# Performance work log

Hardware: AMD Instinct MI355X
Metric: run time of the kernel (lower is better)

## Reference

```python
import jax, jax.numpy as jnp
import numpy as np

B, T, XD, ZD, H = 1024, 1000, 8, 8, 256


def setup_inputs() -> dict:
    key = jax.random.key(0)
    ks = jax.random.split(key, 10)
    # monotonically increasing time grid, identical per batch element: [B, T, 1]
    t = jnp.broadcast_to(jnp.linspace(0.0, 10.0, T, dtype=jnp.float32)[None, :, None], (B, T, 1))
    x = jax.random.normal(ks[0], (B, T, XD), jnp.float32)
    z = jax.random.normal(ks[1], (B, T, ZD), jnp.float32)
    event_t = jax.random.uniform(ks[2], (B, 1), jnp.float32, 3.0, 7.0)
    z_jump = jax.random.normal(ks[3], (B, ZD), jnp.float32)
    in_dim = 3 * (XD + ZD)

    def lin(k, fan_in, fan_out):
        return jax.random.normal(k, (fan_in, fan_out), jnp.float32) * (1.0 / np.sqrt(fan_in))

    W1 = lin(ks[4], in_dim, H); b1 = jnp.zeros((H,), jnp.float32)
    W2 = lin(ks[5], H, H);     b2 = jnp.zeros((H,), jnp.float32)
    W3 = lin(ks[6], H, H);     b3 = jnp.zeros((H,), jnp.float32)
    W4 = lin(ks[7], H, XD);    b4 = jnp.zeros((XD,), jnp.float32)
    return dict(t=t, x=x, z=z, event_t=event_t, z_jump=z_jump,
                W1=W1, b1=b1, W2=W2, b2=b2, W3=W3, b3=b3, W4=W4, b4=b4)


def reference(t, x, z, event_t, z_jump, W1, b1, W2, b2, W3, b3, W4, b4):
    # all_initial = cat(x[:,0], z[:,0]) : [B, XD+ZD]
    all_initial = jnp.concatenate([x[:, 0], z[:, 0]], axis=-1)

    def de_func(x_cur, z_eff):
        xtzt = jnp.concatenate([x_cur, z_eff], axis=-1)                      # [B, XD+ZD]
        inp = jnp.concatenate([all_initial, xtzt - all_initial, xtzt], -1)   # [B, 3*(XD+ZD)]
        h = jax.nn.elu(inp @ W1 + b1)
        h = jax.nn.elu(h @ W2 + b2)
        h = jax.nn.elu(h @ W3 + b3)
        return h @ W4 + b4                                                   # [B, XD]

    t_seq = jnp.moveaxis(t, 1, 0)   # [T, B, 1]
    z_seq = jnp.moveaxis(z, 1, 0)   # [T, B, ZD]
    dt = t_seq[1:] - t_seq[:-1]     # [T-1, B, 1]

    def step(x_cur, step_in):
        t_i, dt_i, z_i = step_in
        # event: once t passes event_t, exogenous z jumps to z_jump
        z_eff = jnp.where(t_i >= event_t, z_jump, z_i)
        x_next = x_cur + dt_i * de_func(x_cur, z_eff)  # explicit Euler step
        return x_next, x_next

    x0 = x[:, 0]  # initial condition [B, XD]
    _, xs = jax.lax.scan(step, x0, (t_seq[:-1], dt, z_seq[:-1]))
    sol = jnp.concatenate([x0[None], xs], axis=0)  # [T, B, XD]
    return jnp.moveaxis(sol, 0, 1)                 # [B, T, XD]
```

## Files before the change

kernel.cpp:

```cpp
#include <hip/hip_runtime.h>
#include <cstdint>
#include <cstddef>

typedef __bf16 bf16x8 __attribute__((ext_vector_type(8)));
typedef float f32x4 __attribute__((ext_vector_type(4)));

#define HD 256
#define TLEN 1000
#define NSTEP 999

#define W1R_OFF 0
#define W2R_OFF 16384
#define W3R_OFF 81920
#define W4R_OFF 147456
#define WS_ELEMS 151552

__device__ __forceinline__ void wg_barrier() {
  asm volatile("s_waitcnt lgkmcnt(0)\n\ts_barrier" ::: "memory");
}

__global__ void prep_weights(const float* __restrict__ W1, const float* __restrict__ b1,
                             const float* __restrict__ W2, const float* __restrict__ W3,
                             const float* __restrict__ W4, __bf16* __restrict__ ws) {
  int tid = blockIdx.x * blockDim.x + threadIdx.x;
  if (tid >= WS_ELEMS) return;
  float val = 0.0f;
  if (tid < W2R_OFF) {
    int t = tid;
    int j = t & 7, lane = (t >> 3) & 63, tt = (t >> 9) & 1, kb = (t >> 10) & 1, w = (t >> 11) & 7;
    int k = kb * 32 + ((lane >> 4) * 8) + j;
    int n = w * 32 + tt * 16 + (lane & 15);
    if (k < 48) val = W1[k * HD + n];
    else if (k == 48) val = b1[n];
  } else if (tid < W3R_OFF) {
    int t = tid - W2R_OFF;
    int j = t & 7, lane = (t >> 3) & 63, tt = (t >> 9) & 1, kb = (t >> 10) & 7, w = (t >> 13) & 7;
    int k = kb * 32 + ((lane >> 4) * 8) + j;
    int n = w * 32 + tt * 16 + (lane & 15);
    val = W2[k * HD + n];
  } else if (tid < W4R_OFF) {
    int t = tid - W3R_OFF;
    int j = t & 7, lane = (t >> 3) & 63, tt = (t >> 9) & 1, kb = (t >> 10) & 7, w = (t >> 13) & 7;
    int k = kb * 32 + ((lane >> 4) * 8) + j;
    int n = w * 32 + tt * 16 + (lane & 15);
    val = W3[k * HD + n];
  } else {
    int t = tid - W4R_OFF;
    int j = t & 7, lane = (t >> 3) & 63, kb = (t >> 9) & 7;
    int k = kb * 32 + ((lane >> 4) * 8) + j;
    int n = lane & 15;
    val = (n < 8) ? W4[k * 8 + n] : 0.0f;
  }
  ws[tid] = (__bf16)val;
}

__global__ __launch_bounds__(512, 2) void ode_main(
    const float* __restrict__ t_g, const float* __restrict__ x_g,
    const float* __restrict__ z_g, const float* __restrict__ ev_g,
    const float* __restrict__ zj_g, const float* __restrict__ b2_g,
    const float* __restrict__ b3_g, const float* __restrict__ b4_g,
    const __bf16* __restrict__ ws, float* __restrict__ out) {
  __shared__ __align__(16) __bf16 h_a[16 * 264];
  __shared__ __align__(16) __bf16 h_b[16 * 264];
  __shared__ __align__(16) float p4[8 * 16 * 8];
  __shared__ __align__(16) float x_cur[16 * 12];
  __shared__ __align__(16) float z_eff[16 * 12];
  __shared__ __align__(16) float x0s[16 * 12];
  __shared__ __align__(16) float z0s[16 * 12];
  __shared__ __align__(16) float zjs[16 * 12];
  __shared__ float evs[16];

  const int tid  = threadIdx.x;
  const int lane = tid & 63;
  const int wid  = tid >> 6;
  const int bcol = lane & 15;
  const int q    = lane >> 4;
  const int b0   = blockIdx.x * 16;

  if (tid < 128) {
    int m = tid >> 3, d = tid & 7;
    size_t gb = (size_t)(b0 + m);
    float x0 = x_g[gb * (TLEN * 8) + d];
    float z0 = z_g[gb * (TLEN * 8) + d];
    x0s[m * 12 + d] = x0;
    z0s[m * 12 + d] = z0;
    x_cur[m * 12 + d] = x0;
    zjs[m * 12 + d] = zj_g[gb * 8 + d];
    out[gb * (TLEN * 8) + d] = x0;
    if (d == 0) evs[m] = ev_g[gb];
  }
  __syncthreads();

  if (tid < 128) {
    int m = tid >> 3, d = tid & 7;
    float t0 = t_g[0];
    z_eff[m * 12 + d] = (t0 >= evs[m]) ? zjs[m * 12 + d] : z0s[m * 12 + d];
  }

  const bf16x8* wsv = (const bf16x8*)ws;
  bf16x8 w1f[2][2], w2f[8][2], w3f[8][2];
#pragma unroll
  for (int kb = 0; kb < 2; ++kb)
#pragma unroll
    for (int tt = 0; tt < 2; ++tt)
      w1f[kb][tt] = wsv[(W1R_OFF / 8) + ((wid * 2 + kb) * 2 + tt) * 64 + lane];
#pragma unroll
  for (int kb = 0; kb < 8; ++kb)
#pragma unroll
    for (int tt = 0; tt < 2; ++tt) {
      w2f[kb][tt] = wsv[(W2R_OFF / 8) + ((wid * 8 + kb) * 2 + tt) * 64 + lane];
      w3f[kb][tt] = wsv[(W3R_OFF / 8) + ((wid * 8 + kb) * 2 + tt) * 64 + lane];
    }
  bf16x8 w4f = wsv[(W4R_OFF / 8) + wid * 64 + lane];

  f32x4 b2v[2], b3v[2];
#pragma unroll
  for (int tt = 0; tt < 2; ++tt) {
    int n0 = wid * 32 + tt * 16 + q * 4;
    b2v[tt] = *(const f32x4*)(b2_g + n0);
    b3v[tt] = *(const f32x4*)(b3_g + n0);
  }
  float b4l = (tid < 128) ? b4_g[tid & 7] : 0.0f;

  const int m1 = lane >> 2;
  const int d0 = (lane & 3) * 2;
  float2 zjf = make_float2(0.f, 0.f);
  float ev1 = 0.f;
  if (wid == 2) {
    zjf.x = zjs[m1 * 12 + d0];
    zjf.y = zjs[m1 * 12 + d0 + 1];
    ev1 = evs[m1];
  }

  f32x4 sub0, sub1;
  bf16x8 a0c;
  {
    const float* base = ((q & 1) ? z0s : x0s) + bcol * 12;
    f32x4 r0 = *(const f32x4*)(base);
    f32x4 r1 = *(const f32x4*)(base + 4);
    sub0 = r0; sub1 = r1;
#pragma unroll
    for (int e = 0; e < 4; ++e) { a0c[e] = (__bf16)r0[e]; a0c[e + 4] = (__bf16)r1[e]; }
  }
  bf16x8 zf;
#pragma unroll
  for (int e = 0; e < 8; ++e) zf[e] = (__bf16)0.f;
  bf16x8 k48f = zf;
  k48f[0] = (__bf16)1.0f;

  __syncthreads();

  float tc = t_g[0];

  auto layer = [&](const __bf16* src, __bf16* dst, const bf16x8 (*wf)[2], const f32x4* bv) {
    bf16x8 bfr[8];
    const bf16x8* hp = (const bf16x8*)src;
#pragma unroll
    for (int kb = 0; kb < 8; ++kb) bfr[kb] = hp[bcol * 33 + kb * 4 + q];
#pragma unroll
    for (int tt = 0; tt < 2; ++tt) {
      f32x4 c = bv[tt];
#pragma unroll
      for (int kb = 0; kb < 8; ++kb)
        c = __builtin_amdgcn_mfma_f32_16x16x32_bf16(wf[kb][tt], bfr[kb], c, 0, 0, 0);
      union { __bf16 h4[4]; unsigned long long u; } pk;
#pragma unroll
      for (int e = 0; e < 4; ++e) {
        float v = c[e];
        v = (v > 0.f) ? v : (__expf(v) - 1.0f);
        pk.h4[e] = (__bf16)v;
      }
      *(unsigned long long*)(dst + bcol * 264 + wid * 32 + tt * 16 + q * 4) = pk.u;
    }
  };

#pragma unroll 1
  for (int i = 0; i < NSTEP; ++i) {
    float tn = t_g[i + 1];
    float2 zpre = make_float2(0.f, 0.f);
    if (wid == 2)
      zpre = *(const float2*)(z_g + ((size_t)(b0 + m1) * TLEN + (i + 1)) * 8 + d0);

    {
      const float* rp = ((q & 1) ? z_eff : x_cur) + bcol * 12;
      f32x4 r0 = *(const f32x4*)(rp);
      f32x4 r1 = *(const f32x4*)(rp + 4);
      bf16x8 f0, f1;
      if (q < 2) {
        f0 = a0c;
#pragma unroll
        for (int e = 0; e < 4; ++e) { f1[e] = (__bf16)r0[e]; f1[e + 4] = (__bf16)r1[e]; }
      } else {
#pragma unroll
        for (int e = 0; e < 4; ++e) {
          f0[e] = (__bf16)(r0[e] - sub0[e]);
          f0[e + 4] = (__bf16)(r1[e] - sub1[e]);
        }
        f1 = (q == 2) ? k48f : zf;
      }
#pragma unroll
      for (int tt = 0; tt < 2; ++tt) {
        f32x4 c = {0.f, 0.f, 0.f, 0.f};
        c = __builtin_amdgcn_mfma_f32_16x16x32_bf16(w1f[0][tt], f0, c, 0, 0, 0);
        c = __builtin_amdgcn_mfma_f32_16x16x32_bf16(w1f[1][tt], f1, c, 0, 0, 0);
        union { __bf16 h4[4]; unsigned long long u; } pk;
#pragma unroll
        for (int e = 0; e < 4; ++e) {
          float v = c[e];
          v = (v > 0.f) ? v : (__expf(v) - 1.0f);
          pk.h4[e] = (__bf16)v;
        }
        *(unsigned long long*)(h_a + bcol * 264 + wid * 32 + tt * 16 + q * 4) = pk.u;
      }
    }
    wg_barrier();
    layer(h_a, h_b, w2f, b2v);
    wg_barrier();
    layer(h_b, h_a, w3f, b3v);

    {
      const bf16x8* hp = (const bf16x8*)h_a;
      bf16x8 h4 = hp[bcol * 33 + wid * 4 + q];
      f32x4 c = {0.f, 0.f, 0.f, 0.f};
      c = __builtin_amdgcn_mfma_f32_16x16x32_bf16(w4f, h4, c, 0, 0, 0);
      if (q < 2)
        *(f32x4*)(p4 + wid * 128 + bcol * 8 + q * 4) = c;
    }
    wg_barrier();

    float dt = tn - tc;
    if (tid < 128) {
      int m = tid >> 3, d = tid & 7;
      float s = b4l;
#pragma unroll
      for (int j = 0; j < 8; ++j) s += p4[j * 128 + m * 8 + d];
      float xn = x_cur[m * 12 + d] + dt * s;
      x_cur[m * 12 + d] = xn;
      out[(size_t)(b0 + m) * (TLEN * 8) + (size_t)(i + 1) * 8 + d] = xn;
    } else if (wid == 2) {
      bool jmp = (tn >= ev1);
      float2 zev = make_float2(jmp ? zjf.x : zpre.x, jmp ? zjf.y : zpre.y);
      *(float2*)(z_eff + m1 * 12 + d0) = zev;
    }
    tc = tn;
    wg_barrier();
  }
}

extern "C" void kernel_launch(void* const* d_in, const int* in_sizes, int n_in,
                              void* d_out, int out_size, void* d_ws, size_t ws_size,
                              hipStream_t stream) {
  const float* t  = (const float*)d_in[0];
  const float* x  = (const float*)d_in[1];
  const float* z  = (const float*)d_in[2];
  const float* ev = (const float*)d_in[3];
  const float* zj = (const float*)d_in[4];
  const float* W1 = (const float*)d_in[5];
  const float* b1 = (const float*)d_in[6];
  const float* W2 = (const float*)d_in[7];
  const float* b2 = (const float*)d_in[8];
  const float* W3 = (const float*)d_in[9];
  const float* b3 = (const float*)d_in[10];
  const float* W4 = (const float*)d_in[11];
  const float* b4 = (const float*)d_in[12];
  __bf16* ws = (__bf16*)d_ws;
  float* out = (float*)d_out;

  prep_weights<<<592, 256, 0, stream>>>(W1, b1, W2, W3, W4, ws);
  ode_main<<<64, 512, 0, stream>>>(t, x, z, ev, zj, b2, b3, b4, ws, out);
}
```

Before: 1.764 ms.

## Remove per-step reduction barrier via LDS atomic accumulation and deferred Euler update

Replaces the p4 partial-sum buffer and its extra barrier with workgroup-scoped LDS atomic adds into an accumulator, and defers the Euler update of x so that it is computed on the fly in the next step's first layer and committed during layer 2. This cuts the per-step barrier count from four to three. It also precomputes z_eff and its delta as packed bf16, splits the MFMA accumulation chains into two independent accumulators, and uses packed bf16 conversion. The costs are LDS atomics on the critical path and slightly more register use.

```diff
diff --git a/kernel.cpp b/kernel.cpp
--- a/kernel.cpp
+++ b/kernel.cpp
@@ -17,6 +17,23 @@
 
 __device__ __forceinline__ void wg_barrier() {
   asm volatile("s_waitcnt lgkmcnt(0)\n\ts_barrier" ::: "memory");
+}
+
+__device__ __forceinline__ uint32_t pk2bf(float a, float b) {
+#if __has_builtin(__builtin_amdgcn_cvt_pk_bf16_f32)
+  typedef __bf16 bf16x2 __attribute__((ext_vector_type(2)));
+  union { bf16x2 v; uint32_t u; } cv;
+  cv.v = __builtin_amdgcn_cvt_pk_bf16_f32(a, b);
+  return cv.u;
+#else
+  union { __bf16 h[2]; uint32_t u; } cv;
+  cv.h[0] = (__bf16)a; cv.h[1] = (__bf16)b;
+  return cv.u;
+#endif
+}
+
+__device__ __forceinline__ float elu(float v) {
+  return v > 0.f ? v : (__expf(v) - 1.0f);
 }
 
 __global__ void prep_weights(const float* __restrict__ W1, const float* __restrict__ b1,
@@ -62,9 +79,10 @@
     const __bf16* __restrict__ ws, float* __restrict__ out) {
   __shared__ __align__(16) __bf16 h_a[16 * 264];
   __shared__ __align__(16) __bf16 h_b[16 * 264];
-  __shared__ __align__(16) float p4[8 * 16 * 8];
-  __shared__ __align__(16) float x_cur[16 * 12];
-  __shared__ __align__(16) float z_eff[16 * 12];
+  __shared__ __align__(16) float x_prev[16 * 12];
+  __shared__ __align__(16) float facc[16 * 12];
+  __shared__ __align__(16) __bf16 zpk[16 * 8];
+  __shared__ __align__(16) __bf16 zdpk[16 * 8];
   __shared__ __align__(16) float x0s[16 * 12];
   __shared__ __align__(16) float z0s[16 * 12];
   __shared__ __align__(16) float zjs[16 * 12];
@@ -82,20 +100,21 @@
     size_t gb = (size_t)(b0 + m);
     float x0 = x_g[gb * (TLEN * 8) + d];
     float z0 = z_g[gb * (TLEN * 8) + d];
+    float zj = zj_g[gb * 8 + d];
+    float ev = ev_g[gb];
     x0s[m * 12 + d] = x0;
     z0s[m * 12 + d] = z0;
-    x_cur[m * 12 + d] = x0;
-    zjs[m * 12 + d] = zj_g[gb * 8 + d];
+    zjs[m * 12 + d] = zj;
+    x_prev[m * 12 + d] = x0;
+    facc[m * 12 + d] = 0.f;
+    float t0 = t_g[0];
+    float ze = (t0 >= ev) ? zj : z0;
+    zpk[m * 8 + d]  = (__bf16)ze;
+    zdpk[m * 8 + d] = (__bf16)(ze - z0);
     out[gb * (TLEN * 8) + d] = x0;
-    if (d == 0) evs[m] = ev_g[gb];
+    if (d == 0) evs[m] = ev;
   }
   __syncthreads();
-
-  if (tid < 128) {
-    int m = tid >> 3, d = tid & 7;
-    float t0 = t_g[0];
-    z_eff[m * 12 + d] = (t0 >= evs[m]) ? zjs[m * 12 + d] : z0s[m * 12 + d];
-  }
 
   const bf16x8* wsv = (const bf16x8*)ws;
   bf16x8 w1f[2][2], w2f[8][2], w3f[8][2];
@@ -120,15 +139,16 @@
     b2v[tt] = *(const f32x4*)(b2_g + n0);
     b3v[tt] = *(const f32x4*)(b3_g + n0);
   }
-  float b4l = (tid < 128) ? b4_g[tid & 7] : 0.0f;
+  f32x4 b4q = {0.f, 0.f, 0.f, 0.f};
+  if (wid == 0 && q < 2) b4q = *(const f32x4*)(b4_g + q * 4);
 
   const int m1 = lane >> 2;
   const int d0 = (lane & 3) * 2;
-  float2 zjf = make_float2(0.f, 0.f);
+  float2 zjf = make_float2(0.f, 0.f), z0f = make_float2(0.f, 0.f);
   float ev1 = 0.f;
   if (wid == 2) {
-    zjf.x = zjs[m1 * 12 + d0];
-    zjf.y = zjs[m1 * 12 + d0 + 1];
+    zjf.x = zjs[m1 * 12 + d0];  zjf.y = zjs[m1 * 12 + d0 + 1];
+    z0f.x = z0s[m1 * 12 + d0];  z0f.y = z0s[m1 * 12 + d0 + 1];
     ev1 = evs[m1];
   }
 
@@ -139,8 +159,10 @@
     f32x4 r0 = *(const f32x4*)(base);
     f32x4 r1 = *(const f32x4*)(base + 4);
     sub0 = r0; sub1 = r1;
-#pragma unroll
-    for (int e = 0; e < 4; ++e) { a0c[e] = (__bf16)r0[e]; a0c[e + 4] = (__bf16)r1[e]; }
+    union { uint32_t u[4]; bf16x8 v; } cv;
+    cv.u[0] = pk2bf(r0[0], r0[1]); cv.u[1] = pk2bf(r0[2], r0[3]);
+    cv.u[2] = pk2bf(r1[0], r1[1]); cv.u[3] = pk2bf(r1[2], r1[3]);
+    a0c = cv.v;
   }
   bf16x8 zf;
 #pragma unroll
@@ -150,7 +172,8 @@
 
   __syncthreads();
 
-  float tc = t_g[0];
+  float tcur = t_g[0];
+  float dtp = 0.f;
 
   auto layer = [&](const __bf16* src, __bf16* dst, const bf16x8 (*wf)[2], const f32x4* bv) {
     bf16x8 bfr[8];
@@ -159,18 +182,17 @@
     for (int kb = 0; kb < 8; ++kb) bfr[kb] = hp[bcol * 33 + kb * 4 + q];
 #pragma unroll
     for (int tt = 0; tt < 2; ++tt) {
-      f32x4 c = bv[tt];
-#pragma unroll
-      for (int kb = 0; kb < 8; ++kb)
-        c = __builtin_amdgcn_mfma_f32_16x16x32_bf16(wf[kb][tt], bfr[kb], c, 0, 0, 0);
-      union { __bf16 h4[4]; unsigned long long u; } pk;
-#pragma unroll
-      for (int e = 0; e < 4; ++e) {
-        float v = c[e];
-        v = (v > 0.f) ? v : (__expf(v) - 1.0f);
-        pk.h4[e] = (__bf16)v;
+      f32x4 cA = bv[tt];
+      f32x4 cB = {0.f, 0.f, 0.f, 0.f};
+#pragma unroll
+      for (int kb = 0; kb < 4; ++kb) {
+        cA = __builtin_amdgcn_mfma_f32_16x16x32_bf16(wf[kb][tt], bfr[kb], cA, 0, 0, 0);
+        cB = __builtin_amdgcn_mfma_f32_16x16x32_bf16(wf[kb + 4][tt], bfr[kb + 4], cB, 0, 0, 0);
       }
-      *(unsigned long long*)(dst + bcol * 264 + wid * 32 + tt * 16 + q * 4) = pk.u;
+      union { uint32_t u[2]; unsigned long long ull; } o;
+      o.u[0] = pk2bf(elu(cA[0] + cB[0]), elu(cA[1] + cB[1]));
+      o.u[1] = pk2bf(elu(cA[2] + cB[2]), elu(cA[3] + cB[3]));
+      *(unsigned long long*)(dst + bcol * 264 + wid * 32 + tt * 16 + q * 4) = o.ull;
     }
   };
 
@@ -182,68 +204,101 @@
       zpre = *(const float2*)(z_g + ((size_t)(b0 + m1) * TLEN + (i + 1)) * 8 + d0);
 
     {
-      const float* rp = ((q & 1) ? z_eff : x_cur) + bcol * 12;
-      f32x4 r0 = *(const f32x4*)(rp);
-      f32x4 r1 = *(const f32x4*)(rp + 4);
       bf16x8 f0, f1;
-      if (q < 2) {
-        f0 = a0c;
-#pragma unroll
-        for (int e = 0; e < 4; ++e) { f1[e] = (__bf16)r0[e]; f1[e + 4] = (__bf16)r1[e]; }
+      if ((q & 1) == 0) {
+        const float* xb = x_prev + bcol * 12;
+        const float* fb = facc + bcol * 12;
+        f32x4 xpA = *(const f32x4*)(xb);
+        f32x4 xpB = *(const f32x4*)(xb + 4);
+        f32x4 fA = *(const f32x4*)(fb);
+        f32x4 fB = *(const f32x4*)(fb + 4);
+        float xc[8];
+#pragma unroll
+        for (int e = 0; e < 4; ++e) {
+          xc[e] = xpA[e] + dtp * fA[e];
+          xc[e + 4] = xpB[e] + dtp * fB[e];
+        }
+        union { uint32_t u[4]; bf16x8 v; } cv;
+        if (q == 0) {
+          cv.u[0] = pk2bf(xc[0], xc[1]); cv.u[1] = pk2bf(xc[2], xc[3]);
+          cv.u[2] = pk2bf(xc[4], xc[5]); cv.u[3] = pk2bf(xc[6], xc[7]);
+          f0 = a0c; f1 = cv.v;
+        } else {
+          cv.u[0] = pk2bf(xc[0] - sub0[0], xc[1] - sub0[1]);
+          cv.u[1] = pk2bf(xc[2] - sub0[2], xc[3] - sub0[3]);
+          cv.u[2] = pk2bf(xc[4] - sub1[0], xc[5] - sub1[1]);
+          cv.u[3] = pk2bf(xc[6] - sub1[2], xc[7] - sub1[3]);
+          f0 = cv.v; f1 = k48f;
+        }
       } else {
-#pragma unroll
-        for (int e = 0; e < 4; ++e) {
-          f0[e] = (__bf16)(r0[e] - sub0[e]);
-          f0[e + 4] = (__bf16)(r1[e] - sub1[e]);
-        }
-        f1 = (q == 2) ? k48f : zf;
+        const __bf16* zb = ((q == 1) ? zpk : zdpk) + bcol * 8;
+        bf16x8 rd = *(const bf16x8*)zb;
+        if (q == 1) { f0 = a0c; f1 = rd; }
+        else        { f0 = rd;  f1 = zf; }
       }
 #pragma unroll
       for (int tt = 0; tt < 2; ++tt) {
         f32x4 c = {0.f, 0.f, 0.f, 0.f};
         c = __builtin_amdgcn_mfma_f32_16x16x32_bf16(w1f[0][tt], f0, c, 0, 0, 0);
         c = __builtin_amdgcn_mfma_f32_16x16x32_bf16(w1f[1][tt], f1, c, 0, 0, 0);
-        union { __bf16 h4[4]; unsigned long long u; } pk;
-#pragma unroll
-        for (int e = 0; e < 4; ++e) {
-          float v = c[e];
-          v = (v > 0.f) ? v : (__expf(v) - 1.0f);
-          pk.h4[e] = (__bf16)v;
-        }
-        *(unsigned long long*)(h_a + bcol * 264 + wid * 32 + tt * 16 + q * 4) = pk.u;
+        union { uint32_t u[2]; unsigned long long ull; } o;
+        o.u[0] = pk2bf(elu(c[0]), elu(c[1]));
+        o.u[1] = pk2bf(elu(c[2]), elu(c[3]));
+        *(unsigned long long*)(h_a + bcol * 264 + wid * 32 + tt * 16 + q * 4) = o.ull;
       }
     }
     wg_barrier();
+
     layer(h_a, h_b, w2f, b2v);
+    if (wid == 0 && q < 2) {
+      float* xb = x_prev + bcol * 12 + q * 4;
+      float* fb = facc + bcol * 12 + q * 4;
+      f32x4 xp = *(const f32x4*)xb;
+      f32x4 fv = *(const f32x4*)fb;
+      f32x4 xn;
+#pragma unroll
+      for (int e = 0; e < 4; ++e) xn[e] = xp[e] + dtp * fv[e];
+      *(f32x4*)xb = xn;
+      *(f32x4*)fb = b4q;
+      *(f32x4*)(out + (size_t)(b0 + bcol) * (TLEN * 8) + (size_t)i * 8 + q * 4) = xn;
+    }
     wg_barrier();
+
     layer(h_b, h_a, w3f, b3v);
-
     {
       const bf16x8* hp = (const bf16x8*)h_a;
       bf16x8 h4 = hp[bcol * 33 + wid * 4 + q];
       f32x4 c = {0.f, 0.f, 0.f, 0.f};
       c = __builtin_amdgcn_mfma_f32_16x16x32_bf16(w4f, h4, c, 0, 0, 0);
-      if (q < 2)
-        *(f32x4*)(p4 + wid * 128 + bcol * 8 + q * 4) = c;
+      if (q < 2) {
+        float* fp = facc + bcol * 12 + q * 4;
+#pragma unroll
+        for (int e = 0; e < 4; ++e)
+          __hip_atomic_fetch_add(fp + e, c[e], __ATOMIC_RELAXED, __HIP_MEMORY_SCOPE_WORKGROUP);
+      }
+    }
+    if (wid == 2) {
+      bool jmp = (tn >= ev1);
+      float za = jmp ? zjf.x : zpre.x;
+      float zb = jmp ? zjf.y : zpre.y;
+      *(uint32_t*)(zpk + m1 * 8 + d0)  = pk2bf(za, zb);
+      *(uint32_t*)(zdpk + m1 * 8 + d0) = pk2bf(za - z0f.x, zb - z0f.y);
     }
     wg_barrier();
 
-    float dt = tn - tc;
-    if (tid < 128) {
-      int m = tid >> 3, d = tid & 7;
-      float s = b4l;
-#pragma unroll
-      for (int j = 0; j < 8; ++j) s += p4[j * 128 + m * 8 + d];
-      float xn = x_cur[m * 12 + d] + dt * s;
-      x_cur[m * 12 + d] = xn;
-      out[(size_t)(b0 + m) * (TLEN * 8) + (size_t)(i + 1) * 8 + d] = xn;
-    } else if (wid == 2) {
-      bool jmp = (tn >= ev1);
-      float2 zev = make_float2(jmp ? zjf.x : zpre.x, jmp ? zjf.y : zpre.y);
-      *(float2*)(z_eff + m1 * 12 + d0) = zev;
-    }
-    tc = tn;
-    wg_barrier();
+    dtp = tn - tcur;
+    tcur = tn;
+  }
+
+  if (wid == 0 && q < 2) {
+    const float* xb = x_prev + bcol * 12 + q * 4;
+    const float* fb = facc + bcol * 12 + q * 4;
+    f32x4 xp = *(const f32x4*)xb;
+    f32x4 fv = *(const f32x4*)fb;
+    f32x4 xn;
+#pragma unroll
+    for (int e = 0; e < 4; ++e) xn[e] = xp[e] + dtp * fv[e];
+    *(f32x4*)(out + (size_t)(b0 + bcol) * (TLEN * 8) + (size_t)NSTEP * 8 + q * 4) = xn;
   }
 }
 
```

After: 3.211 ms. +82.1%, slower.
